# Kernel tuning notes

Hardware: AMD Instinct MI355X
Metric: run time of the kernel (lower is better)

Reference implementation:

```python
import jax, jax.numpy as jnp
import numpy as np


def setup_inputs() -> dict:
    key = jax.random.key(0)
    kq, kk, kv = jax.random.split(key, 3)
    B, L, E = 16, 2048, 512
    return {
        "queries": jax.random.normal(kq, (B, L, E), dtype=jnp.float32),
        "keys": jax.random.normal(kk, (B, L, E), dtype=jnp.float32),
        "values": jax.random.normal(kv, (B, L, E), dtype=jnp.float32),
    }


def reference(queries, keys, values):
    # queries: [B, L, E], keys: [B, S, E], values: [B, S, D]; causal mask requires L == S
    B, L, E = queries.shape
    S = keys.shape[1]
    scale = 1.0 / np.float32(np.sqrt(E))  # self.scale is None -> 1/sqrt(E)
    scores = jnp.einsum('ble,bse->bls', queries, keys)  # [B, L, S]
    causal = jnp.triu(jnp.ones((L, S), dtype=bool), k=1)  # True above diagonal -> masked
    scores = jnp.where(causal, -jnp.inf, scores)
    A = jax.nn.softmax(scale * scores, axis=-1)  # dropout p=0.0 -> identity
    V = jnp.einsum('bls,bsd->bld', A, values)  # [B, L, D]
    return V
```

## Files before the change

### kernel.cpp

```cpp
#include <hip/hip_runtime.h>
#include <hip/hip_bf16.h>

typedef __attribute__((ext_vector_type(8))) short short8;
typedef __attribute__((ext_vector_type(4))) float f32x4;
typedef __attribute__((ext_vector_type(4))) unsigned short us4;

#define NB 16
#define L_ 2048
#define E_ 512
#define SCALE 0.04419417382415922f

static __device__ __forceinline__ unsigned short f2bf(float f) {
  return __builtin_bit_cast(unsigned short, __float2bfloat16(f));
}

__global__ void __launch_bounds__(256)
convert_k(const float* __restrict__ K, unsigned short* __restrict__ Kb, int n4) {
  int i = blockIdx.x * 256 + threadIdx.x;
  const int stride = gridDim.x * 256;
  for (; i < n4; i += stride) {
    f32x4 v = ((const f32x4*)K)[i];
    us4 u;
    u[0] = f2bf(v[0]); u[1] = f2bf(v[1]); u[2] = f2bf(v[2]); u[3] = f2bf(v[3]);
    ((us4*)Kb)[i] = u;
  }
}

__global__ void __launch_bounds__(256)
transpose_v(const float* __restrict__ V, unsigned short* __restrict__ VT) {
  __shared__ unsigned short Lt[64][66];
  const int b   = (int)blockIdx.x;
  const int bz  = b >> 8;
  const int t8  = b & 255;
  const int ts  = (t8 >> 3) * 64;
  const int td  = (t8 & 7) * 64;
  const float* Vb = V + (size_t)bz * (L_ * E_);
  unsigned short* VTb = VT + (size_t)bz * (E_ * L_);
  const int tid = threadIdx.x;
  const int dq  = tid & 15;
  const int s4  = tid >> 4;
#pragma unroll
  for (int i = 0; i < 4; ++i) {
    const int s = s4 + i * 16;
    f32x4 v = *(const f32x4*)(Vb + (size_t)(ts + s) * E_ + td + dq * 4);
#pragma unroll
    for (int j = 0; j < 4; ++j) Lt[dq * 4 + j][s] = f2bf(v[j]);
  }
  __syncthreads();
  const int c  = tid & 63;
  const int r0 = tid >> 6;
#pragma unroll
  for (int i = 0; i < 16; ++i) {
    const int d = r0 + i * 4;
    VTb[(size_t)(td + d) * L_ + ts + c] = Lt[d][c];
  }
}

__global__ void __launch_bounds__(512)
fattn_bf16(const float* __restrict__ Q, const unsigned short* __restrict__ Kb,
           const unsigned short* __restrict__ VT, float* __restrict__ O) {
  __shared__ __align__(16) unsigned short Qs[32][512];
  __shared__ __align__(16) unsigned short P2[2][16][32][8];
  __shared__ float lsum[32][8];

  const int tid  = threadIdx.x;
  const int w    = tid >> 6;
  const int lane = tid & 63;
  const int g    = lane >> 4;
  const int ln   = lane & 15;
  const int bid  = (int)blockIdx.x;
  const int bz   = bid & 15;
  const int q0   = (63 - (bid >> 4)) * 32;
  const int d0   = w * 64;

  const float* Qb = Q + (size_t)bz * (L_ * E_);
  const unsigned short* Kbb = Kb + (size_t)bz * (L_ * E_);
  const unsigned short* VTb = VT + (size_t)bz * (E_ * L_);

  {
    const int row = tid >> 4;
    const int c0  = (tid & 15) * 32;
    const float* qp = Qb + (size_t)(q0 + row) * E_ + c0;
    char* rowbase = (char*)&Qs[row][0];
#pragma unroll
    for (int j = 0; j < 4; ++j) {
      f32x4 a = *(const f32x4*)(qp + j * 8);
      f32x4 b = *(const f32x4*)(qp + j * 8 + 4);
      short8 t;
      t[0] = (short)f2bf(a[0] * SCALE); t[1] = (short)f2bf(a[1] * SCALE);
      t[2] = (short)f2bf(a[2] * SCALE); t[3] = (short)f2bf(a[3] * SCALE);
      t[4] = (short)f2bf(b[0] * SCALE); t[5] = (short)f2bf(b[1] * SCALE);
      t[6] = (short)f2bf(b[2] * SCALE); t[7] = (short)f2bf(b[3] * SCALE);
      const int byteoff = ((c0 + j * 8) * 2) ^ ((row & 7) << 4);
      *(short8*)(rowbase + byteoff) = t;
    }
  }

  f32x4 acc[2][4];
#pragma unroll
  for (int mt = 0; mt < 2; ++mt)
#pragma unroll
    for (int n = 0; n < 4; ++n) acc[mt][n] = (f32x4){0.f, 0.f, 0.f, 0.f};
  float l_part[2] = {0.f, 0.f};

  __syncthreads();

  const int nIter = q0 / 128 + 1;
  for (int it = 0; it < nIter; ++it) {
    const int s0   = it * 128;
    const int sw   = s0 + w * 16;
    const bool last = (it == nIter - 1);
    const bool dead = (sw > q0 + 31);

    f32x4 ps[2];
    ps[0] = (f32x4){0.f, 0.f, 0.f, 0.f};
    ps[1] = (f32x4){0.f, 0.f, 0.f, 0.f};
    if (!dead) {
      const unsigned short* kp = Kbb + (size_t)(sw + ln) * E_ + g * 8;
      short8 k0 = *(const short8*)(kp + 0 * 32);
      short8 k1 = *(const short8*)(kp + 1 * 32);
      short8 k2 = *(const short8*)(kp + 2 * 32);
      short8 k3 = *(const short8*)(kp + 3 * 32);
      short8 k4 = *(const short8*)(kp + 4 * 32);
      short8 k5 = *(const short8*)(kp + 5 * 32);
      short8 k6 = *(const short8*)(kp + 6 * 32);
      short8 k7 = *(const short8*)(kp + 7 * 32);
#define QKSTEP(KR, KC)                                                         \
      {                                                                        \
        const int qoff = ((KC) * 64 + g * 16) ^ ((ln & 7) << 4);               \
        short8 qa0 = *(const short8*)((const char*)&Qs[ln][0] + qoff);         \
        short8 qa1 = *(const short8*)((const char*)&Qs[16 + ln][0] + qoff);    \
        ps[0] = __builtin_amdgcn_mfma_f32_16x16x32_bf16(KR, qa0, ps[0], 0, 0, 0); \
        ps[1] = __builtin_amdgcn_mfma_f32_16x16x32_bf16(KR, qa1, ps[1], 0, 0, 0); \
      }
      QKSTEP(k0, 0);  k0 = *(const short8*)(kp + 8 * 32);
      QKSTEP(k1, 1);  k1 = *(const short8*)(kp + 9 * 32);
      QKSTEP(k2, 2);  k2 = *(const short8*)(kp + 10 * 32);
      QKSTEP(k3, 3);  k3 = *(const short8*)(kp + 11 * 32);
      QKSTEP(k4, 4);  k4 = *(const short8*)(kp + 12 * 32);
      QKSTEP(k5, 5);  k5 = *(const short8*)(kp + 13 * 32);
      QKSTEP(k6, 6);  k6 = *(const short8*)(kp + 14 * 32);
      QKSTEP(k7, 7);  k7 = *(const short8*)(kp + 15 * 32);
      QKSTEP(k0, 8);  QKSTEP(k1, 9);  QKSTEP(k2, 10); QKSTEP(k3, 11);
      QKSTEP(k4, 12); QKSTEP(k5, 13); QKSTEP(k6, 14); QKSTEP(k7, 15);
#undef QKSTEP
    }

    const int buf = it & 1;
#pragma unroll
    for (int mt = 0; mt < 2; ++mt) {
      us4 u;
#pragma unroll
      for (int r = 0; r < 4; ++r) {
        const int s_g = sw + g * 4 + r;
        const bool msk = last && (s_g > q0 + mt * 16 + ln);
        const float p = msk ? 0.f : __expf(ps[mt][r]);
        l_part[mt] += p;
        u[r] = f2bf(p);
      }
      *(us4*)&P2[buf][2 * w + (g >> 1)][mt * 16 + ln][(g & 1) * 4] = u;
    }

    const unsigned short* vp0 = VTb + (size_t)(d0 + 0 * 16 + ln) * L_ + s0 + g * 8;
    const unsigned short* vp1 = VTb + (size_t)(d0 + 1 * 16 + ln) * L_ + s0 + g * 8;
    const unsigned short* vp2 = VTb + (size_t)(d0 + 2 * 16 + ln) * L_ + s0 + g * 8;
    const unsigned short* vp3 = VTb + (size_t)(d0 + 3 * 16 + ln) * L_ + s0 + g * 8;
    short8 vA = *(const short8*)(vp0);
    short8 vB = *(const short8*)(vp1);
    short8 vC = *(const short8*)(vp2);
    short8 vD = *(const short8*)(vp3);

    __syncthreads();

#define PVKC(KC, RELOAD)                                                       \
    {                                                                          \
      short8 pa0 = *(const short8*)&P2[buf][(KC) * 4 + g][ln][0];              \
      short8 pa1 = *(const short8*)&P2[buf][(KC) * 4 + g][16 + ln][0];         \
      acc[0][0] = __builtin_amdgcn_mfma_f32_16x16x32_bf16(pa0, vA, acc[0][0], 0, 0, 0); \
      acc[1][0] = __builtin_amdgcn_mfma_f32_16x16x32_bf16(pa1, vA, acc[1][0], 0, 0, 0); \
      if (RELOAD) vA = *(const short8*)(vp0 + ((KC) + 1) * 32);                \
      acc[0][1] = __builtin_amdgcn_mfma_f32_16x16x32_bf16(pa0, vB, acc[0][1], 0, 0, 0); \
      acc[1][1] = __builtin_amdgcn_mfma_f32_16x16x32_bf16(pa1, vB, acc[1][1], 0, 0, 0); \
      if (RELOAD) vB = *(const short8*)(vp1 + ((KC) + 1) * 32);                \
      acc[0][2] = __builtin_amdgcn_mfma_f32_16x16x32_bf16(pa0, vC, acc[0][2], 0, 0, 0); \
      acc[1][2] = __builtin_amdgcn_mfma_f32_16x16x32_bf16(pa1, vC, acc[1][2], 0, 0, 0); \
      if (RELOAD) vC = *(const short8*)(vp2 + ((KC) + 1) * 32);                \
      acc[0][3] = __builtin_amdgcn_mfma_f32_16x16x32_bf16(pa0, vD, acc[0][3], 0, 0, 0); \
      acc[1][3] = __builtin_amdgcn_mfma_f32_16x16x32_bf16(pa1, vD, acc[1][3], 0, 0, 0); \
      if (RELOAD) vD = *(const short8*)(vp3 + ((KC) + 1) * 32);                \
    }
    PVKC(0, true);
    PVKC(1, true);
    PVKC(2, true);
    PVKC(3, false);
#undef PVKC
  }

#pragma unroll
  for (int mt = 0; mt < 2; ++mt) {
    l_part[mt] += __shfl_xor(l_part[mt], 16);
    l_part[mt] += __shfl_xor(l_part[mt], 32);
  }
  if (lane < 16) {
    lsum[ln][w]      = l_part[0];
    lsum[16 + ln][w] = l_part[1];
  }
  __syncthreads();

  float* Ob = O + (size_t)bz * (L_ * E_);
#pragma unroll
  for (int mt = 0; mt < 2; ++mt) {
    float inv[4];
#pragma unroll
    for (int r = 0; r < 4; ++r) {
      f32x4 u = *(const f32x4*)&lsum[mt * 16 + g * 4 + r][0];
      f32x4 v2 = *(const f32x4*)&lsum[mt * 16 + g * 4 + r][4];
      inv[r] = 1.0f / (u[0] + u[1] + u[2] + u[3] + v2[0] + v2[1] + v2[2] + v2[3]);
    }
#pragma unroll
    for (int n = 0; n < 4; ++n) {
      const int col = d0 + n * 16 + ln;
#pragma unroll
      for (int r = 0; r < 4; ++r)
        Ob[(size_t)(q0 + mt * 16 + g * 4 + r) * E_ + col] = acc[mt][n][r] * inv[r];
    }
  }
}

__global__ void __launch_bounds__(512)
fattn_fallback(const float* __restrict__ Q, const float* __restrict__ K,
               const float* __restrict__ V, float* __restrict__ O) {
  __shared__ __align__(16) unsigned short Qs[32][512];
  __shared__ __align__(16) unsigned short P2[2][16][33][8];
  __shared__ float lsum[32][8];

  const int tid  = threadIdx.x;
  const int w    = tid >> 6;
  const int lane = tid & 63;
  const int g    = lane >> 4;
  const int ln   = lane & 15;
  const int bid  = (int)blockIdx.x;
  const int bz   = bid & 15;
  const int q0   = (63 - (bid >> 4)) * 32;
  const int d0   = w * 64;

  const float* Qb = Q + (size_t)bz * (L_ * E_);
  const float* Kb2 = K + (size_t)bz * (L_ * E_);
  const float* Vb = V + (size_t)bz * (L_ * E_);

  {
    const int row = tid >> 4;
    const int c0  = (tid & 15) * 32;
    const float* qp = Qb + (size_t)(q0 + row) * E_ + c0;
    char* rowbase = (char*)&Qs[row][0];
#pragma unroll
    for (int j = 0; j < 4; ++j) {
      f32x4 a = *(const f32x4*)(qp + j * 8);
      f32x4 b = *(const f32x4*)(qp + j * 8 + 4);
      short8 t;
      t[0] = (short)f2bf(a[0] * SCALE); t[1] = (short)f2bf(a[1] * SCALE);
      t[2] = (short)f2bf(a[2] * SCALE); t[3] = (short)f2bf(a[3] * SCALE);
      t[4] = (short)f2bf(b[0] * SCALE); t[5] = (short)f2bf(b[1] * SCALE);
      t[6] = (short)f2bf(b[2] * SCALE); t[7] = (short)f2bf(b[3] * SCALE);
      const int byteoff = ((c0 + j * 8) * 2) ^ ((row & 7) << 4);
      *(short8*)(rowbase + byteoff) = t;
    }
  }

  f32x4 acc[2][4];
#pragma unroll
  for (int mt = 0; mt < 2; ++mt)
#pragma unroll
    for (int n = 0; n < 4; ++n) acc[mt][n] = (f32x4){0.f, 0.f, 0.f, 0.f};
  float l_part[2][4];
#pragma unroll
  for (int mt = 0; mt < 2; ++mt)
#pragma unroll
    for (int r = 0; r < 4; ++r) l_part[mt][r] = 0.f;

  __syncthreads();

  const int nIter = q0 / 128 + 1;
  for (int it = 0; it < nIter; ++it) {
    const int s0   = it * 128;
    const int sw   = s0 + w * 16;
    const bool last = (it == nIter - 1);
    const bool dead = (sw > q0 + 31);

    f32x4 ps[2];
    ps[0] = (f32x4){0.f, 0.f, 0.f, 0.f};
    ps[1] = (f32x4){0.f, 0.f, 0.f, 0.f};
    if (!dead) {
      const float* kp = Kb2 + (size_t)(sw + ln) * E_ + g * 8;
#pragma unroll
      for (int kc = 0; kc < 16; ++kc) {
        f32x4 a = *(const f32x4*)(kp + kc * 32);
        f32x4 b = *(const f32x4*)(kp + kc * 32 + 4);
        short8 kf;
        kf[0] = (short)f2bf(a[0]); kf[1] = (short)f2bf(a[1]);
        kf[2] = (short)f2bf(a[2]); kf[3] = (short)f2bf(a[3]);
        kf[4] = (short)f2bf(b[0]); kf[5] = (short)f2bf(b[1]);
        kf[6] = (short)f2bf(b[2]); kf[7] = (short)f2bf(b[3]);
        const int qoff = (kc * 64 + g * 16) ^ ((ln & 7) << 4);
        short8 qa0 = *(const short8*)((const char*)&Qs[ln][0] + qoff);
        short8 qa1 = *(const short8*)((const char*)&Qs[16 + ln][0] + qoff);
        ps[0] = __builtin_amdgcn_mfma_f32_16x16x32_bf16(qa0, kf, ps[0], 0, 0, 0);
        ps[1] = __builtin_amdgcn_mfma_f32_16x16x32_bf16(qa1, kf, ps[1], 0, 0, 0);
      }
    }

    const int buf = it & 1;
    const int bucket = w * 2 + (ln >> 3);
    const int elem = ln & 7;
#pragma unroll
    for (int mt = 0; mt < 2; ++mt)
#pragma unroll
      for (int r = 0; r < 4; ++r) {
        const bool msk = dead || (last && (sw + ln > q0 + mt * 16 + g * 4 + r));
        const float p = msk ? 0.f : __expf(ps[mt][r]);
        l_part[mt][r] += p;
        P2[buf][bucket][mt * 16 + g * 4 + r][elem] = f2bf(p);
      }
    __syncthreads();

    const int kcMax = last ? ((q0 + 31 - s0) >> 5) + 1 : 4;
    for (int kc = 0; kc < kcMax; ++kc) {
      short8 pa0 = *(const short8*)&P2[buf][kc * 4 + g][ln][0];
      short8 pa1 = *(const short8*)&P2[buf][kc * 4 + g][16 + ln][0];
#pragma unroll
      for (int n = 0; n < 4; ++n) {
        const float* vp = Vb + (size_t)(s0 + kc * 32 + g * 8) * E_ + d0 + n * 16 + ln;
        float vr[8];
#pragma unroll
        for (int i = 0; i < 8; ++i) vr[i] = vp[(size_t)i * E_];
        short8 vf;
#pragma unroll
        for (int i = 0; i < 8; ++i) vf[i] = (short)f2bf(vr[i]);
        acc[0][n] = __builtin_amdgcn_mfma_f32_16x16x32_bf16(pa0, vf, acc[0][n], 0, 0, 0);
        acc[1][n] = __builtin_amdgcn_mfma_f32_16x16x32_bf16(pa1, vf, acc[1][n], 0, 0, 0);
      }
    }
  }

#pragma unroll
  for (int mt = 0; mt < 2; ++mt)
#pragma unroll
    for (int r = 0; r < 4; ++r)
#pragma unroll
      for (int off = 1; off < 16; off <<= 1)
        l_part[mt][r] += __shfl_xor(l_part[mt][r], off);
  if (ln == 0) {
#pragma unroll
    for (int mt = 0; mt < 2; ++mt)
#pragma unroll
      for (int r = 0; r < 4; ++r)
        lsum[mt * 16 + g * 4 + r][w] = l_part[mt][r];
  }
  __syncthreads();

  float* Ob = O + (size_t)bz * (L_ * E_);
#pragma unroll
  for (int mt = 0; mt < 2; ++mt) {
    float inv[4];
#pragma unroll
    for (int r = 0; r < 4; ++r) {
      f32x4 u = *(const f32x4*)&lsum[mt * 16 + g * 4 + r][0];
      f32x4 v2 = *(const f32x4*)&lsum[mt * 16 + g * 4 + r][4];
      inv[r] = 1.0f / (u[0] + u[1] + u[2] + u[3] + v2[0] + v2[1] + v2[2] + v2[3]);
    }
#pragma unroll
    for (int n = 0; n < 4; ++n) {
      const int col = d0 + n * 16 + ln;
#pragma unroll
      for (int r = 0; r < 4; ++r)
        Ob[(size_t)(q0 + mt * 16 + g * 4 + r) * E_ + col] = acc[mt][n][r] * inv[r];
    }
  }
}

extern "C" void kernel_launch(void* const* d_in, const int* in_sizes, int n_in,
                              void* d_out, int out_size, void* d_ws, size_t ws_size,
                              hipStream_t stream) {
  const float* Q = (const float*)d_in[0];
  const float* K = (const float*)d_in[1];
  const float* V = (const float*)d_in[2];
  float* O = (float*)d_out;
  const size_t elems = (size_t)NB * L_ * E_;
  if (ws_size >= elems * 4) {
    unsigned short* Kb = (unsigned short*)d_ws;
    unsigned short* VT = Kb + elems;
    convert_k<<<dim3(2048), 256, 0, stream>>>(K, Kb, (int)(elems / 4));
    transpose_v<<<dim3(4096), 256, 0, stream>>>(V, VT);
    fattn_bf16<<<dim3(1024), 512, 0, stream>>>(Q, Kb, VT, O);
  } else {
    fattn_fallback<<<dim3(1024), 512, 0, stream>>>(Q, K, V, O);
  }
}
```

Before: 300.3 us.

## Prefetch next-tile K and V fragments across loop iterations, drop dead-warp skip

Software-pipelines the flash-attention loop: the first K and V fragments are loaded before the loop, and each iteration issues loads for the next tile's K rows and V columns while the current MFMAs run. This hides global-load latency at iteration boundaries. The dead-warp skip is removed, so warps whose keys lie wholly above the diagonal now compute QK anyway (results are masked). The change also pins waves_per_eu to 4 and adds a sched_barrier, which may raise register pressure or constrain scheduling.

```diff
diff --git a/kernel.cpp b/kernel.cpp
--- a/kernel.cpp
+++ b/kernel.cpp
@@ -57,6 +57,7 @@
 }
 
 __global__ void __launch_bounds__(512)
+__attribute__((amdgpu_waves_per_eu(4, 4)))
 fattn_bf16(const float* __restrict__ Q, const unsigned short* __restrict__ Kb,
            const unsigned short* __restrict__ VT, float* __restrict__ O) {
   __shared__ __align__(16) unsigned short Qs[32][512];
@@ -103,6 +104,24 @@
     for (int n = 0; n < 4; ++n) acc[mt][n] = (f32x4){0.f, 0.f, 0.f, 0.f};
   float l_part[2] = {0.f, 0.f};
 
+  const unsigned short* kp = Kbb + (size_t)(w * 16 + ln) * E_ + g * 8;
+  short8 k0 = *(const short8*)(kp + 0 * 32);
+  short8 k1 = *(const short8*)(kp + 1 * 32);
+  short8 k2 = *(const short8*)(kp + 2 * 32);
+  short8 k3 = *(const short8*)(kp + 3 * 32);
+  short8 k4 = *(const short8*)(kp + 4 * 32);
+  short8 k5 = *(const short8*)(kp + 5 * 32);
+  short8 k6 = *(const short8*)(kp + 6 * 32);
+  short8 k7 = *(const short8*)(kp + 7 * 32);
+  const unsigned short* vpA = VTb + (size_t)(d0 + 0 * 16 + ln) * L_ + g * 8;
+  const unsigned short* vpB = VTb + (size_t)(d0 + 1 * 16 + ln) * L_ + g * 8;
+  const unsigned short* vpC = VTb + (size_t)(d0 + 2 * 16 + ln) * L_ + g * 8;
+  const unsigned short* vpD = VTb + (size_t)(d0 + 3 * 16 + ln) * L_ + g * 8;
+  short8 vA = *(const short8*)(vpA);
+  short8 vB = *(const short8*)(vpB);
+  short8 vC = *(const short8*)(vpC);
+  short8 vD = *(const short8*)(vpD);
+
   __syncthreads();
 
   const int nIter = q0 / 128 + 1;
@@ -110,41 +129,39 @@
     const int s0   = it * 128;
     const int sw   = s0 + w * 16;
     const bool last = (it == nIter - 1);
-    const bool dead = (sw > q0 + 31);
+    const unsigned short* kpn = Kbb + (size_t)(((sw + 128) & 2047) + ln) * E_ + g * 8;
+    const int scn = (s0 + 128) & 2047;
 
     f32x4 ps[2];
     ps[0] = (f32x4){0.f, 0.f, 0.f, 0.f};
     ps[1] = (f32x4){0.f, 0.f, 0.f, 0.f};
-    if (!dead) {
-      const unsigned short* kp = Kbb + (size_t)(sw + ln) * E_ + g * 8;
-      short8 k0 = *(const short8*)(kp + 0 * 32);
-      short8 k1 = *(const short8*)(kp + 1 * 32);
-      short8 k2 = *(const short8*)(kp + 2 * 32);
-      short8 k3 = *(const short8*)(kp + 3 * 32);
-      short8 k4 = *(const short8*)(kp + 4 * 32);
-      short8 k5 = *(const short8*)(kp + 5 * 32);
-      short8 k6 = *(const short8*)(kp + 6 * 32);
-      short8 k7 = *(const short8*)(kp + 7 * 32);
 #define QKSTEP(KR, KC)                                                         \
-      {                                                                        \
-        const int qoff = ((KC) * 64 + g * 16) ^ ((ln & 7) << 4);               \
-        short8 qa0 = *(const short8*)((const char*)&Qs[ln][0] + qoff);         \
-        short8 qa1 = *(const short8*)((const char*)&Qs[16 + ln][0] + qoff);    \
-        ps[0] = __builtin_amdgcn_mfma_f32_16x16x32_bf16(KR, qa0, ps[0], 0, 0, 0); \
-        ps[1] = __builtin_amdgcn_mfma_f32_16x16x32_bf16(KR, qa1, ps[1], 0, 0, 0); \
-      }
-      QKSTEP(k0, 0);  k0 = *(const short8*)(kp + 8 * 32);
-      QKSTEP(k1, 1);  k1 = *(const short8*)(kp + 9 * 32);
-      QKSTEP(k2, 2);  k2 = *(const short8*)(kp + 10 * 32);
-      QKSTEP(k3, 3);  k3 = *(const short8*)(kp + 11 * 32);
-      QKSTEP(k4, 4);  k4 = *(const short8*)(kp + 12 * 32);
-      QKSTEP(k5, 5);  k5 = *(const short8*)(kp + 13 * 32);
-      QKSTEP(k6, 6);  k6 = *(const short8*)(kp + 14 * 32);
-      QKSTEP(k7, 7);  k7 = *(const short8*)(kp + 15 * 32);
-      QKSTEP(k0, 8);  QKSTEP(k1, 9);  QKSTEP(k2, 10); QKSTEP(k3, 11);
-      QKSTEP(k4, 12); QKSTEP(k5, 13); QKSTEP(k6, 14); QKSTEP(k7, 15);
+    {                                                                          \
+      const int qoff = ((KC) * 64 + g * 16) ^ ((ln & 7) << 4);                 \
+      short8 qa0 = *(const short8*)((const char*)&Qs[ln][0] + qoff);           \
+      short8 qa1 = *(const short8*)((const char*)&Qs[16 + ln][0] + qoff);      \
+      ps[0] = __builtin_amdgcn_mfma_f32_16x16x32_bf16(KR, qa0, ps[0], 0, 0, 0); \
+      ps[1] = __builtin_amdgcn_mfma_f32_16x16x32_bf16(KR, qa1, ps[1], 0, 0, 0); \
+    }
+    QKSTEP(k0, 0);  k0 = *(const short8*)(kp + 8 * 32);
+    QKSTEP(k1, 1);  k1 = *(const short8*)(kp + 9 * 32);
+    QKSTEP(k2, 2);  k2 = *(const short8*)(kp + 10 * 32);
+    QKSTEP(k3, 3);  k3 = *(const short8*)(kp + 11 * 32);
+    QKSTEP(k4, 4);  k4 = *(const short8*)(kp + 12 * 32);
+    QKSTEP(k5, 5);  k5 = *(const short8*)(kp + 13 * 32);
+    QKSTEP(k6, 6);  k6 = *(const short8*)(kp + 14 * 32);
+    QKSTEP(k7, 7);  k7 = *(const short8*)(kp + 15 * 32);
+    QKSTEP(k0, 8);  k0 = *(const short8*)(kpn + 0 * 32);
+    QKSTEP(k1, 9);  k1 = *(const short8*)(kpn + 1 * 32);
+    QKSTEP(k2, 10); k2 = *(const short8*)(kpn + 2 * 32);
+    QKSTEP(k3, 11); k3 = *(const short8*)(kpn + 3 * 32);
+    QKSTEP(k4, 12); k4 = *(const short8*)(kpn + 4 * 32);
+    QKSTEP(k5, 13); k5 = *(const short8*)(kpn + 5 * 32);
+    QKSTEP(k6, 14); k6 = *(const short8*)(kpn + 6 * 32);
+    QKSTEP(k7, 15); k7 = *(const short8*)(kpn + 7 * 32);
 #undef QKSTEP
-    }
+    __builtin_amdgcn_sched_barrier(0);
+    kp = kpn;
 
     const int buf = it & 1;
 #pragma unroll
@@ -161,38 +178,29 @@
       *(us4*)&P2[buf][2 * w + (g >> 1)][mt * 16 + ln][(g & 1) * 4] = u;
     }
 
-    const unsigned short* vp0 = VTb + (size_t)(d0 + 0 * 16 + ln) * L_ + s0 + g * 8;
-    const unsigned short* vp1 = VTb + (size_t)(d0 + 1 * 16 + ln) * L_ + s0 + g * 8;
-    const unsigned short* vp2 = VTb + (size_t)(d0 + 2 * 16 + ln) * L_ + s0 + g * 8;
-    const unsigned short* vp3 = VTb + (size_t)(d0 + 3 * 16 + ln) * L_ + s0 + g * 8;
-    short8 vA = *(const short8*)(vp0);
-    short8 vB = *(const short8*)(vp1);
-    short8 vC = *(const short8*)(vp2);
-    short8 vD = *(const short8*)(vp3);
-
     __syncthreads();
 
-#define PVKC(KC, RELOAD)                                                       \
+#define PVKC(KC, OFF)                                                          \
     {                                                                          \
       short8 pa0 = *(const short8*)&P2[buf][(KC) * 4 + g][ln][0];              \
       short8 pa1 = *(const short8*)&P2[buf][(KC) * 4 + g][16 + ln][0];         \
       acc[0][0] = __builtin_amdgcn_mfma_f32_16x16x32_bf16(pa0, vA, acc[0][0], 0, 0, 0); \
       acc[1][0] = __builtin_amdgcn_mfma_f32_16x16x32_bf16(pa1, vA, acc[1][0], 0, 0, 0); \
-      if (RELOAD) vA = *(const short8*)(vp0 + ((KC) + 1) * 32);                \
+      vA = *(const short8*)(vpA + (OFF));                                      \
       acc[0][1] = __builtin_amdgcn_mfma_f32_16x16x32_bf16(pa0, vB, acc[0][1], 0, 0, 0); \
       acc[1][1] = __builtin_amdgcn_mfma_f32_16x16x32_bf16(pa1, vB, acc[1][1], 0, 0, 0); \
-      if (RELOAD) vB = *(const short8*)(vp1 + ((KC) + 1) * 32);                \
+      vB = *(const short8*)(vpB + (OFF));                                      \
       acc[0][2] = __builtin_amdgcn_mfma_f32_16x16x32_bf16(pa0, vC, acc[0][2], 0, 0, 0); \
       acc[1][2] = __builtin_amdgcn_mfma_f32_16x16x32_bf16(pa1, vC, acc[1][2], 0, 0, 0); \
-      if (RELOAD) vC = *(const short8*)(vp2 + ((KC) + 1) * 32);                \
+      vC = *(const short8*)(vpC + (OFF));                                      \
       acc[0][3] = __builtin_amdgcn_mfma_f32_16x16x32_bf16(pa0, vD, acc[0][3], 0, 0, 0); \
       acc[1][3] = __builtin_amdgcn_mfma_f32_16x16x32_bf16(pa1, vD, acc[1][3], 0, 0, 0); \
-      if (RELOAD) vD = *(const short8*)(vp3 + ((KC) + 1) * 32);                \
-    }
-    PVKC(0, true);
-    PVKC(1, true);
-    PVKC(2, true);
-    PVKC(3, false);
+      vD = *(const short8*)(vpD + (OFF));                                      \
+    }
+    PVKC(0, s0 + 32);
+    PVKC(1, s0 + 64);
+    PVKC(2, s0 + 96);
+    PVKC(3, scn);
 #undef PVKC
   }
 
```

After: 360.0 us. 1.2x slower.
